# Kernel optimization log

Measured on AMD Instinct MI355X. Metric: run time of the kernel, lower is better.

Reference implementation:

```python
import jax, jax.numpy as jnp
import numpy as np

N, M, D = 4096, 4096, 8


def setup_inputs() -> dict:
    key = jax.random.key(0)
    k1, k2 = jax.random.split(key)
    x = jax.random.normal(k1, (N, D), dtype=jnp.float32)
    xx = jax.random.normal(k2, (M, D), dtype=jnp.float32)
    # parameters stored in free (log) form; positive() == exp()
    log_scale = jnp.zeros((D,), dtype=jnp.float32)      # scale = 1.0 per dim
    log_variance = jnp.zeros((), dtype=jnp.float32)     # variance = 1.0
    return {"x": x, "xx": xx, "log_scale": log_scale, "log_variance": log_variance}


def reference(x, xx, log_scale, log_variance):
    scale = jnp.exp(log_scale)          # positive(_scale), shape [D]
    variance = jnp.exp(log_variance)    # positive(_variance), scalar (diag())
    # r: [N, M, D] broadcasted, scaled pairwise difference
    r = (x[:, None, :] - xx[None, :, :]) / scale
    # cov: [N, M] RBF kernel matrix
    cov = jnp.exp(-0.5 * jnp.sum(r * r, axis=-1)) * variance
    return cov
```

## Files before the change

kernel.cpp:

```cpp
#include <hip/hip_runtime.h>
#include <math.h>


constexpr int D   = 8;
constexpr int TJ  = 4;
constexpr int TI  = 8;
constexpr int BLK = 256;

typedef float f32x4 __attribute__((ext_vector_type(4)));

__global__ __launch_bounds__(BLK) void rbf_kernel(
    const float* __restrict__ x,
    const float* __restrict__ xx,
    const float* __restrict__ log_scale,
    const float* __restrict__ log_var,
    float* __restrict__ out,
    int N, int M)
{
    const int j0 = (blockIdx.x * BLK + threadIdx.x) * TJ;
    const int i0 = blockIdx.y * TI;
    if (j0 + TJ > M || i0 + TI > N) return;

    float w[D];
#pragma unroll
    for (int d = 0; d < D; ++d) {
        const float s = __expf(-log_scale[d]);
        w[d] = s * s;
    }
    const float lv = log_var[0];

    float B[TJ][D], c[TJ];
#pragma unroll
    for (int jj = 0; jj < TJ; ++jj) {
        const float4* p = (const float4*)(xx + (size_t)(j0 + jj) * D);
        const float4 a = p[0], b = p[1];
        const float v[D] = {a.x, a.y, a.z, a.w, b.x, b.y, b.z, b.w};
        float q = 0.f;
#pragma unroll
        for (int d = 0; d < D; ++d) {
            B[jj][d] = v[d] * w[d];
            q = fmaf(v[d], B[jj][d], q);
        }
        c[jj] = fmaf(-0.5f, q, lv);
    }

#pragma unroll
    for (int r = 0; r < TI; ++r) {
        const int i = i0 + r;
        const float4* px = (const float4*)(x + (size_t)i * D);
        const float4 a = px[0], b = px[1];
        const float v[D] = {a.x, a.y, a.z, a.w, b.x, b.y, b.z, b.w};
        float q = 0.f;
#pragma unroll
        for (int d = 0; d < D; ++d) q = fmaf(v[d] * w[d], v[d], q);
        const float h = -0.5f * q;

        float res[TJ];
#pragma unroll
        for (int jj = 0; jj < TJ; ++jj) {
            float e = h + c[jj];
#pragma unroll
            for (int d = 0; d < D; ++d) e = fmaf(v[d], B[jj][d], e);
            res[jj] = __expf(e);
        }
        const f32x4 o = {res[0], res[1], res[2], res[3]};
        __builtin_nontemporal_store(o, (f32x4*)(out + (size_t)i * M + j0));
    }
}

extern "C" void kernel_launch(void* const* d_in, const int* in_sizes, int n_in,
                              void* d_out, int out_size, void* d_ws, size_t ws_size,
                              hipStream_t stream) {
    const float* x  = (const float*)d_in[0];
    const float* xx = (const float*)d_in[1];
    const float* ls = (const float*)d_in[2];
    const float* lv = (const float*)d_in[3];
    float* out      = (float*)d_out;

    const int N = in_sizes[0] / D;
    const int M = in_sizes[1] / D;

    dim3 block(BLK, 1, 1);
    dim3 grid((M + BLK * TJ - 1) / (BLK * TJ), (N + TI - 1) / TI, 1);
    rbf_kernel<<<grid, block, 0, stream>>>(x, xx, ls, lv, out, N, M);
}
```

Before: 86.74 us.

## Process one output row per block, fold log2e into weights, use plain stores

Each block now computes a single row of the output instead of eight, so each xx point is reloaded and its weighted terms recomputed for every row rather than reused across eight rows. The log2(e) factor is folded into the scale weights and log-variance so the exponent can use the hardware exp2 instruction directly. The nontemporal store is replaced by an ordinary vector store. The grid grows eightfold in y, trading more parallel blocks for redundant xx loads and arithmetic.

Measured after the change: 131.9 us. 52.1% more time.

```diff
diff --git a/kernel.cpp b/kernel.cpp
--- a/kernel.cpp
+++ b/kernel.cpp
@@ -4,7 +4,6 @@
 
 constexpr int D   = 8;
 constexpr int TJ  = 4;
-constexpr int TI  = 8;
 constexpr int BLK = 256;
 
 typedef float f32x4 __attribute__((ext_vector_type(4)));
@@ -17,55 +16,46 @@
     float* __restrict__ out,
     int N, int M)
 {
-    const int j0 = (blockIdx.x * BLK + threadIdx.x) * TJ;
-    const int i0 = blockIdx.y * TI;
-    if (j0 + TJ > M || i0 + TI > N) return;
+    const int j0 = blockIdx.x * (BLK * TJ) + threadIdx.x * TJ;
+    const int i  = blockIdx.y;
+    if (j0 + TJ > M || i >= N) return;
 
+    constexpr float LOG2E = 1.4426950408889634f;
     float w[D];
 #pragma unroll
     for (int d = 0; d < D; ++d) {
         const float s = __expf(-log_scale[d]);
-        w[d] = s * s;
+        w[d] = s * s * LOG2E;
     }
-    const float lv = log_var[0];
+    const float lv2 = log_var[0] * LOG2E;
 
-    float B[TJ][D], c[TJ];
+    const float4* px = (const float4*)(x + (size_t)i * D);
+    const float4 xa = px[0], xb = px[1];
+    const float xv[D] = {xa.x, xa.y, xa.z, xa.w, xb.x, xb.y, xb.z, xb.w};
+    float hq = 0.f;
+#pragma unroll
+    for (int d = 0; d < D; ++d) hq = fmaf(xv[d] * w[d], xv[d], hq);
+    const float h = -0.5f * hq;
+
+    float res[TJ];
 #pragma unroll
     for (int jj = 0; jj < TJ; ++jj) {
         const float4* p = (const float4*)(xx + (size_t)(j0 + jj) * D);
         const float4 a = p[0], b = p[1];
         const float v[D] = {a.x, a.y, a.z, a.w, b.x, b.y, b.z, b.w};
+        float e = h + lv2;
         float q = 0.f;
 #pragma unroll
         for (int d = 0; d < D; ++d) {
-            B[jj][d] = v[d] * w[d];
-            q = fmaf(v[d], B[jj][d], q);
+            const float bd = v[d] * w[d];
+            q = fmaf(v[d], bd, q);
+            e = fmaf(xv[d], bd, e);
         }
-        c[jj] = fmaf(-0.5f, q, lv);
+        res[jj] = __builtin_amdgcn_exp2f(fmaf(-0.5f, q, e));
     }
 
-#pragma unroll
-    for (int r = 0; r < TI; ++r) {
-        const int i = i0 + r;
-        const float4* px = (const float4*)(x + (size_t)i * D);
-        const float4 a = px[0], b = px[1];
-        const float v[D] = {a.x, a.y, a.z, a.w, b.x, b.y, b.z, b.w};
-        float q = 0.f;
-#pragma unroll
-        for (int d = 0; d < D; ++d) q = fmaf(v[d] * w[d], v[d], q);
-        const float h = -0.5f * q;
-
-        float res[TJ];
-#pragma unroll
-        for (int jj = 0; jj < TJ; ++jj) {
-            float e = h + c[jj];
-#pragma unroll
-            for (int d = 0; d < D; ++d) e = fmaf(v[d], B[jj][d], e);
-            res[jj] = __expf(e);
-        }
-        const f32x4 o = {res[0], res[1], res[2], res[3]};
-        __builtin_nontemporal_store(o, (f32x4*)(out + (size_t)i * M + j0));
-    }
+    const f32x4 o = {res[0], res[1], res[2], res[3]};
+    *(f32x4*)(out + (size_t)i * M + j0) = o;
 }
 
 extern "C" void kernel_launch(void* const* d_in, const int* in_sizes, int n_in,
@@ -81,6 +71,6 @@
     const int M = in_sizes[1] / D;
 
     dim3 block(BLK, 1, 1);
-    dim3 grid((M + BLK * TJ - 1) / (BLK * TJ), (N + TI - 1) / TI, 1);
+    dim3 grid((M + BLK * TJ - 1) / (BLK * TJ), N, 1);
     rbf_kernel<<<grid, block, 0, stream>>>(x, xx, ls, lv, out, N, M);
 }
```

## Fold log2e into weights, use exp2, batch row stores, drop nontemporal stores

Applied to the files above, without the earlier changes.

Pre-scales the weights and log-variance by log2(e) so each output needs only a raw hardware exp2 instead of __expf's extra multiply. Each block now covers 16 rows, computed in batches of 8 whose results are held in registers and then written back-to-back. The nontemporal stores become plain stores. The aim is less ALU work per output, better store grouping and fewer blocks re-reading xx, at the cost of more registers and the loss of the cache-bypass hint on a 64 MB output.

New measurement: 86.66 us. No clear change (-0.1%).

```diff
diff --git a/kernel.cpp b/kernel.cpp
--- a/kernel.cpp
+++ b/kernel.cpp
@@ -2,10 +2,11 @@
 #include <math.h>
 
 
-constexpr int D   = 8;
-constexpr int TJ  = 4;
-constexpr int TI  = 8;
-constexpr int BLK = 256;
+constexpr int D    = 8;
+constexpr int TJ   = 4;
+constexpr int BLK  = 256;
+constexpr int RPB  = 16;
+constexpr int RBAT = 8;
 
 typedef float f32x4 __attribute__((ext_vector_type(4)));
 
@@ -17,17 +18,18 @@
     float* __restrict__ out,
     int N, int M)
 {
-    const int j0 = (blockIdx.x * BLK + threadIdx.x) * TJ;
-    const int i0 = blockIdx.y * TI;
-    if (j0 + TJ > M || i0 + TI > N) return;
+    const int j0 = blockIdx.x * (BLK * TJ) + threadIdx.x * TJ;
+    const int i0 = blockIdx.y * RPB;
+    if (j0 + TJ > M || i0 + RPB > N) return;
 
+    constexpr float LOG2E = 1.4426950408889634f;
     float w[D];
 #pragma unroll
     for (int d = 0; d < D; ++d) {
         const float s = __expf(-log_scale[d]);
-        w[d] = s * s;
+        w[d] = s * s * LOG2E;
     }
-    const float lv = log_var[0];
+    const float lv2 = log_var[0] * LOG2E;
 
     float B[TJ][D], c[TJ];
 #pragma unroll
@@ -41,30 +43,38 @@
             B[jj][d] = v[d] * w[d];
             q = fmaf(v[d], B[jj][d], q);
         }
-        c[jj] = fmaf(-0.5f, q, lv);
+        c[jj] = fmaf(-0.5f, q, lv2);
     }
 
 #pragma unroll
-    for (int r = 0; r < TI; ++r) {
-        const int i = i0 + r;
-        const float4* px = (const float4*)(x + (size_t)i * D);
-        const float4 a = px[0], b = px[1];
-        const float v[D] = {a.x, a.y, a.z, a.w, b.x, b.y, b.z, b.w};
-        float q = 0.f;
+    for (int bat = 0; bat < RPB / RBAT; ++bat) {
+        const int ib = i0 + bat * RBAT;
+        float res[RBAT][TJ];
+
 #pragma unroll
-        for (int d = 0; d < D; ++d) q = fmaf(v[d] * w[d], v[d], q);
-        const float h = -0.5f * q;
+        for (int r = 0; r < RBAT; ++r) {
+            const int i = ib + r;
+            const float4* px = (const float4*)(x + (size_t)i * D);
+            const float4 a = px[0], b = px[1];
+            const float xv[D] = {a.x, a.y, a.z, a.w, b.x, b.y, b.z, b.w};
+            float q = 0.f;
+#pragma unroll
+            for (int d = 0; d < D; ++d) q = fmaf(xv[d] * w[d], xv[d], q);
+            const float h = -0.5f * q;
+#pragma unroll
+            for (int jj = 0; jj < TJ; ++jj) {
+                float e = h + c[jj];
+#pragma unroll
+                for (int d = 0; d < D; ++d) e = fmaf(xv[d], B[jj][d], e);
+                res[r][jj] = __builtin_amdgcn_exp2f(e);
+            }
+        }
 
-        float res[TJ];
 #pragma unroll
-        for (int jj = 0; jj < TJ; ++jj) {
-            float e = h + c[jj];
-#pragma unroll
-            for (int d = 0; d < D; ++d) e = fmaf(v[d], B[jj][d], e);
-            res[jj] = __expf(e);
+        for (int r = 0; r < RBAT; ++r) {
+            const f32x4 o = {res[r][0], res[r][1], res[r][2], res[r][3]};
+            *(f32x4*)(out + (size_t)(ib + r) * M + j0) = o;
         }
-        const f32x4 o = {res[0], res[1], res[2], res[3]};
-        __builtin_nontemporal_store(o, (f32x4*)(out + (size_t)i * M + j0));
     }
 }
 
@@ -81,6 +91,6 @@
     const int M = in_sizes[1] / D;
 
     dim3 block(BLK, 1, 1);
-    dim3 grid((M + BLK * TJ - 1) / (BLK * TJ), (N + TI - 1) / TI, 1);
+    dim3 grid((M + BLK * TJ - 1) / (BLK * TJ), (N + RPB - 1) / RPB, 1);
     rbf_kernel<<<grid, block, 0, stream>>>(x, xx, ls, lv, out, N, M);
 }
```
